# Kernel tuning notes

Measured on AMD Instinct MI355X. Metric: run time of the kernel, lower is better.

## Reference

```python
import jax, jax.numpy as jnp
import numpy as np

B, C, H, W = 4, 32, 32, 1024
PATCH = 21           # patch_size in spatial_correlation_sample
DIL = 2              # dilation_patch
PAD = DIL * (PATCH - 1) // 2  # 20: max displacement, zero-padded out-of-range samples


def setup_inputs() -> dict:
    key = jax.random.key(0)
    k1, k2 = jax.random.split(key)
    x1 = jax.random.normal(k1, (B, C, H, W), dtype=jnp.float32)
    x2 = jax.random.normal(k2, (B, C, H, W), dtype=jnp.float32)
    return {"x1": x1, "x2": x2}


def _correlate(x1, x2):
    # spatial_correlation_sample(kernel_size=1, patch_size=21, stride=1,
    #                            padding=0, dilation_patch=2)
    # out[b, pi, pj, h, w] = sum_c x1[b,c,h,w] * x2[b,c,h+2*(pi-10), w+2*(pj-10)]
    # with out-of-bounds x2 samples treated as zero.
    b, c, h, w = x1.shape
    x2p = jnp.pad(x2, ((0, 0), (0, 0), (PAD, PAD), (PAD, PAD)))
    chans = []
    for i in range(PATCH):      # fixed 21x21 displacement grid (static slices)
        for j in range(PATCH):
            win = jax.lax.slice(x2p, (0, 0, DIL * i, DIL * j),
                                (b, c, DIL * i + h, DIL * j + w))
            chans.append(jnp.einsum('bchw,bchw->bhw', x1, win))
    corr = jnp.stack(chans, axis=1) / c  # (b, 441, h, w), normalized by n_channels
    return jax.nn.leaky_relu(corr, negative_slope=0.1)


def reference(x1, x2):
    # CorrelationNetwork.forward returns only out_correlation; the conv/deconv
    # flow pyramid does not contribute to the returned tensor (and the
    # visualize_flow calls reference undefined symbols in the original).
    return _correlate(x1, x2)
```

## Files before the change

### kernel.cpp

```cpp
#include <hip/hip_runtime.h>

#define BB    4
#define CC    32
#define HH    32
#define WW    1024
#define PATCH 21
#define DIL   2
#define RAD   10
#define PADW  20
#define CHUNK 4
#define LROW  (WW + 2*PADW)

template <int PJ0, int TPT>
__device__ __forceinline__ void corr_body(const float* __restrict__ x1,
                                          const float* __restrict__ x2,
                                          float* __restrict__ out,
                                          float* __restrict__ sx2 ) {
    const int tid = threadIdx.x;
    const int h   = blockIdx.x;
    const int bp  = blockIdx.y;
    const int b   = bp / PATCH;
    const int pi  = bp - b * PATCH;
    const int r2  = h + DIL * (pi - RAD);
    const int w4  = tid * 4;

    float* outp = out + (((size_t)(b * PATCH * PATCH + pi * PATCH + PJ0)) * HH + h) * WW + w4;

    if (r2 < 0 || r2 >= HH) {
        float4 z = make_float4(0.f, 0.f, 0.f, 0.f);
#pragma unroll
        for (int j = 0; j < TPT; j++)
            *(float4*)(outp + (size_t)j * HH * WW) = z;
        return;
    }

    const float* x1p = x1 + (((size_t)(b * CC) * HH + h) * WW) + w4;
    const float* x2p = x2 + (((size_t)(b * CC) * HH + r2) * WW);

    float acc[TPT][4];
#pragma unroll
    for (int j = 0; j < TPT; j++)
#pragma unroll
        for (int k = 0; k < 4; k++) acc[j][k] = 0.f;

    for (int cc = 0; cc < CC; cc += CHUNK) {
        __syncthreads();
        for (int idx = tid; idx < CHUNK * (LROW / 4); idx += 256) {
            int c  = idx / (LROW / 4);
            int i4 = idx - c * (LROW / 4);
            int u  = i4 * 4 - PADW;
            float4 v = make_float4(0.f, 0.f, 0.f, 0.f);
            if (u >= 0 && u <= WW - 4)
                v = *(const float4*)(x2p + (size_t)(cc + c) * HH * WW + u);
            *(float4*)&sx2[c * LROW + i4 * 4] = v;
        }
        __syncthreads();

#pragma unroll
        for (int c = 0; c < CHUNK; c++) {
            float4 av = *(const float4*)(x1p + (size_t)(cc + c) * HH * WW);
            const float a[4] = {av.x, av.y, av.z, av.w};

            constexpr int WFL = 4 + 2 * (TPT - 1);
            constexpr int WV  = (WFL + 3) / 4;
            float win[WV * 4];
            const float* wbase = &sx2[c * LROW + w4 + 2 * PJ0];
#pragma unroll
            for (int v = 0; v < WV; v++)
                *(float4*)&win[v * 4] = *(const float4*)(wbase + v * 4);

#pragma unroll
            for (int j = 0; j < TPT; j++)
#pragma unroll
                for (int k = 0; k < 4; k++)
                    acc[j][k] = fmaf(a[k], win[2 * j + k], acc[j][k]);
        }
    }

    const float inv_c = 1.0f / (float)CC;
#pragma unroll
    for (int j = 0; j < TPT; j++) {
        float4 o;
        float* ov = (float*)&o;
#pragma unroll
        for (int k = 0; k < 4; k++) {
            float v = acc[j][k] * inv_c;
            ov[k] = v > 0.f ? v : 0.1f * v;
        }
        *(float4*)(outp + (size_t)j * HH * WW) = o;
    }
}

__global__ __launch_bounds__(256, 8)
void corr_kernel(const float* __restrict__ x1, const float* __restrict__ x2,
                 float* __restrict__ out) {
    __shared__ float sx2[CHUNK * LROW];
    if (blockIdx.z == 0)      corr_body<0, 8>(x1, x2, out, sx2);
    else if (blockIdx.z == 1) corr_body<8, 8>(x1, x2, out, sx2);
    else                      corr_body<16, 5>(x1, x2, out, sx2);
}

extern "C" void kernel_launch(void* const* d_in, const int* in_sizes, int n_in,
                              void* d_out, int out_size, void* d_ws, size_t ws_size,
                              hipStream_t stream) {
    const float* x1 = (const float*)d_in[0];
    const float* x2 = (const float*)d_in[1];
    float* out = (float*)d_out;

    dim3 grid(HH, BB * PATCH, 3);
    dim3 block(256, 1, 1);
    corr_kernel<<<grid, block, 0, stream>>>(x1, x2, out);
}
```

Before: 328.8 us.

## Register-block correlation over two rows and eight columns with even/odd LDS layout

Each block now handles two output rows, and each thread computes eight consecutive columns for 10–11 horizontal displacements. The grid shrinks to half the rows and two displacement groups instead of three. The x2 rows in shared memory are split into even and odd halves, so the stride-2 displacement window becomes contiguous and can be read with aligned float4 loads. This cuts redundant LDS reads and x1 reloads per FMA. In exchange it uses many more accumulator registers (launch bounds drop to 3 blocks) and twice the LDS per block, which lowers occupancy.

```diff
diff --git a/kernel.cpp b/kernel.cpp
--- a/kernel.cpp
+++ b/kernel.cpp
@@ -10,6 +10,8 @@
 #define PADW  20
 #define CHUNK 4
 #define LROW  (WW + 2*PADW)
+#define EHALF (LROW/2)
+#define NG    (LROW/8)
 
 template <int PJ0, int TPT>
 __device__ __forceinline__ void corr_body(const float* __restrict__ x1,
@@ -17,87 +19,111 @@
                                           float* __restrict__ out,
                                           float* __restrict__ sx2 ) {
     const int tid = threadIdx.x;
-    const int h   = blockIdx.x;
+    const int tw  = tid & 127;
+    const int th  = tid >> 7;
+    const int h2  = blockIdx.x;
     const int bp  = blockIdx.y;
     const int b   = bp / PATCH;
     const int pi  = bp - b * PATCH;
-    const int r2  = h + DIL * (pi - RAD);
-    const int w4  = tid * 4;
+    const int r20 = 2 * (h2 + pi - RAD);
+    const int h   = 2 * h2 + th;
+    const int w8  = tw * 8;
 
-    float* outp = out + (((size_t)(b * PATCH * PATCH + pi * PATCH + PJ0)) * HH + h) * WW + w4;
+    float* outp = out + (((size_t)(b * PATCH * PATCH + pi * PATCH + PJ0)) * HH + h) * WW + w8;
 
-    if (r2 < 0 || r2 >= HH) {
+    if ((unsigned)r20 > 30u) {
         float4 z = make_float4(0.f, 0.f, 0.f, 0.f);
 #pragma unroll
-        for (int j = 0; j < TPT; j++)
-            *(float4*)(outp + (size_t)j * HH * WW) = z;
+        for (int j = 0; j < TPT; j++) {
+            *(float4*)(outp + (size_t)j * HH * WW)     = z;
+            *(float4*)(outp + (size_t)j * HH * WW + 4) = z;
+        }
         return;
     }
 
-    const float* x1p = x1 + (((size_t)(b * CC) * HH + h) * WW) + w4;
-    const float* x2p = x2 + (((size_t)(b * CC) * HH + r2) * WW);
-
-    float acc[TPT][4];
+    float acc[TPT][8];
 #pragma unroll
     for (int j = 0; j < TPT; j++)
 #pragma unroll
-        for (int k = 0; k < 4; k++) acc[j][k] = 0.f;
+        for (int k = 0; k < 8; k++) acc[j][k] = 0.f;
+
+    constexpr int D  = PJ0 & 3;
+    constexpr int EB = PJ0 & ~3;
 
     for (int cc = 0; cc < CC; cc += CHUNK) {
         __syncthreads();
-        for (int idx = tid; idx < CHUNK * (LROW / 4); idx += 256) {
-            int c  = idx / (LROW / 4);
-            int i4 = idx - c * (LROW / 4);
-            int u  = i4 * 4 - PADW;
-            float4 v = make_float4(0.f, 0.f, 0.f, 0.f);
-            if (u >= 0 && u <= WW - 4)
-                v = *(const float4*)(x2p + (size_t)(cc + c) * HH * WW + u);
-            *(float4*)&sx2[c * LROW + i4 * 4] = v;
+#pragma unroll
+        for (int t = 0; t < (CHUNK * 2 * NG + 255) / 256; t++) {
+            int idx = tid + t * 256;
+            if (idx < CHUNK * 2 * NG) {
+                int c  = idx / (2 * NG);
+                int r  = idx - c * (2 * NG);
+                int rr = r / NG;
+                int g  = r - rr * NG;
+                int u0 = 8 * g - PADW;
+                const float* src = x2 + ((size_t)(b * CC + cc + c) * HH + (r20 + rr)) * WW;
+                float4 v0 = make_float4(0.f, 0.f, 0.f, 0.f);
+                float4 v1 = v0;
+                if (u0 >= 0     && u0     <= WW - 4) v0 = *(const float4*)(src + u0);
+                if (u0 + 4 >= 0 && u0 + 4 <= WW - 4) v1 = *(const float4*)(src + u0 + 4);
+                float* dst = sx2 + (c * 2 + rr) * LROW + 4 * g;
+                *(float4*)dst           = make_float4(v0.x, v0.z, v1.x, v1.z);
+                *(float4*)(dst + EHALF) = make_float4(v0.y, v0.w, v1.y, v1.w);
+            }
         }
         __syncthreads();
 
 #pragma unroll
-        for (int c = 0; c < CHUNK; c++) {
-            float4 av = *(const float4*)(x1p + (size_t)(cc + c) * HH * WW);
-            const float a[4] = {av.x, av.y, av.z, av.w};
+        for (int cl = 0; cl < CHUNK; cl++) {
+            const float* x1p = x1 + ((size_t)(b * CC + cc + cl) * HH + h) * WW + w8;
+            float4 a0 = *(const float4*)x1p;
+            float4 a1 = *(const float4*)(x1p + 4);
+            const float a[8] = {a0.x, a0.y, a0.z, a0.w, a1.x, a1.y, a1.z, a1.w};
 
-            constexpr int WFL = 4 + 2 * (TPT - 1);
-            constexpr int WV  = (WFL + 3) / 4;
-            float win[WV * 4];
-            const float* wbase = &sx2[c * LROW + w4 + 2 * PJ0];
+            const float* eb = sx2 + (cl * 2 + th) * LROW + 4 * tw + EB;
+            float ef[16], of[16];
 #pragma unroll
-            for (int v = 0; v < WV; v++)
-                *(float4*)&win[v * 4] = *(const float4*)(wbase + v * 4);
-
+            for (int v = 0; v < 4; v++) {
+                *(float4*)&ef[4 * v] = *(const float4*)(eb + 4 * v);
+                *(float4*)&of[4 * v] = *(const float4*)(eb + EHALF + 4 * v);
+            }
 #pragma unroll
             for (int j = 0; j < TPT; j++)
 #pragma unroll
-                for (int k = 0; k < 4; k++)
-                    acc[j][k] = fmaf(a[k], win[2 * j + k], acc[j][k]);
+                for (int k = 0; k < 8; k++) {
+                    float wv = (k & 1) ? of[D + j + (k >> 1)] : ef[D + j + (k >> 1)];
+                    acc[j][k] = fmaf(a[k], wv, acc[j][k]);
+                }
         }
     }
 
     const float inv_c = 1.0f / (float)CC;
 #pragma unroll
     for (int j = 0; j < TPT; j++) {
-        float4 o;
-        float* ov = (float*)&o;
+        float4 o0, o1;
+        float* p0 = (float*)&o0;
+        float* p1 = (float*)&o1;
 #pragma unroll
         for (int k = 0; k < 4; k++) {
             float v = acc[j][k] * inv_c;
-            ov[k] = v > 0.f ? v : 0.1f * v;
+            p0[k] = v > 0.f ? v : 0.1f * v;
         }
-        *(float4*)(outp + (size_t)j * HH * WW) = o;
+#pragma unroll
+        for (int k = 0; k < 4; k++) {
+            float v = acc[j][4 + k] * inv_c;
+            p1[k] = v > 0.f ? v : 0.1f * v;
+        }
+        *(float4*)(outp + (size_t)j * HH * WW)     = o0;
+        *(float4*)(outp + (size_t)j * HH * WW + 4) = o1;
     }
 }
 
-__global__ __launch_bounds__(256, 8)
+__global__ __launch_bounds__(256, 3)
 void corr_kernel(const float* __restrict__ x1, const float* __restrict__ x2,
                  float* __restrict__ out) {
-    __shared__ float sx2[CHUNK * LROW];
-    if (blockIdx.z == 0)      corr_body<0, 8>(x1, x2, out, sx2);
-    else if (blockIdx.z == 1) corr_body<8, 8>(x1, x2, out, sx2);
-    else                      corr_body<16, 5>(x1, x2, out, sx2);
+    __shared__ float sx2[CHUNK * 2 * LROW];
+    if (blockIdx.z == 0) corr_body<0, 11>(x1, x2, out, sx2);
+    else                 corr_body<11, 10>(x1, x2, out, sx2);
 }
 
 extern "C" void kernel_launch(void* const* d_in, const int* in_sizes, int n_in,
@@ -107,7 +133,7 @@
     const float* x2 = (const float*)d_in[1];
     float* out = (float*)d_out;
 
-    dim3 grid(HH, BB * PATCH, 3);
+    dim3 grid(HH / 2, BB * PATCH, 2);
     dim3 block(256, 1, 1);
     corr_kernel<<<grid, block, 0, stream>>>(x1, x2, out);
 }
```

After: 569.3 us. +73.1%, slower.
